# Performance work log

Hardware: AMD Instinct MI355X
Metric: run time of the kernel (lower is better)

The kernel has to match this reference:

```python
import jax, jax.numpy as jnp
import numpy as np

B, S, D = 2, 2048, 1024
H, DH = 16, 64
EPS = 1e-5

def setup_inputs() -> dict:
    key = jax.random.key(0)
    ks = jax.random.split(key, 8)
    s = 0.02
    return {
        "x": jax.random.normal(ks[0], (B, S, D), dtype=jnp.float32),
        "ln_gamma": jnp.ones((D,), jnp.float32),
        "ln_beta": jnp.zeros((D,), jnp.float32),
        "wq": jax.random.normal(ks[1], (D, H * DH), jnp.float32) * s,
        "bq": jnp.zeros((H * DH,), jnp.float32),
        "wk": jax.random.normal(ks[2], (D, H * DH), jnp.float32) * s,
        "bk": jnp.zeros((H * DH,), jnp.float32),
        "wv": jax.random.normal(ks[3], (D, H * DH), jnp.float32) * s,
        "bv": jnp.zeros((H * DH,), jnp.float32),
        "wo": jax.random.normal(ks[4], (H * DH, D), jnp.float32) * s,
        "bo": jnp.zeros((D,), jnp.float32),
    }

def reference(x, ln_gamma, ln_beta, wq, bq, wk, bk, wv, bv, wo, bo):
    # Pre-LayerNorm over d_model
    mu = jnp.mean(x, axis=-1, keepdims=True)
    var = jnp.var(x, axis=-1, keepdims=True)
    xn = (x - mu) * jax.lax.rsqrt(var + EPS) * ln_gamma + ln_beta

    b, s, _ = xn.shape
    q = (xn @ wq + bq).reshape(b, s, H, DH)
    k = (xn @ wk + bk).reshape(b, s, H, DH)
    v = (xn @ wv + bv).reshape(b, s, H, DH)

    scale = jnp.sqrt(jnp.float32(DH))
    scores = jnp.einsum('bihd,bjhd->bhij', q, k) / scale  # [b,h,s,s]
    att = jax.nn.softmax(scores, axis=-1)
    out = jnp.einsum('bhij,bjhd->bihd', att, v).reshape(b, s, H * DH)
    return out @ wo + bo
```

## Files before the change

### kernel.cpp

```cpp
#include <hip/hip_runtime.h>
#include <math.h>

#define SEQ   2048
#define DM    1024
#define NHEAD 16
#define HD    64
#define NTOK  4096
#define EPS   1e-5f
#define SCALE_C 0.18033688f

typedef __attribute__((ext_vector_type(8))) short v8s;
typedef __attribute__((ext_vector_type(4))) float v4f;
typedef unsigned short ushort_t;

#define GLOAD16(g, l) __builtin_amdgcn_global_load_lds( \
    (const __attribute__((address_space(1))) unsigned int*)(g), \
    (__attribute__((address_space(3))) unsigned int*)(l), 16, 0, 0)

__device__ __forceinline__ unsigned short f2bf(float f) {
  union { float f; unsigned u; } v; v.f = f;
  unsigned r = v.u + 0x7FFFu + ((v.u >> 16) & 1u);
  return (unsigned short)(r >> 16);
}

__device__ __forceinline__ unsigned pack2_bf16(float a, float b) {
  union { float f; unsigned u; } ua, ub;
  ua.f = a; ub.f = b;
  return __builtin_amdgcn_perm(ub.u + 0x8000u, ua.u + 0x8000u, 0x07060302u);
}

__global__ __launch_bounds__(256) void prep_kernel(
    const float* __restrict__ x, const float* __restrict__ g,
    const float* __restrict__ be, ushort_t* __restrict__ y,
    const float* __restrict__ w0, const float* __restrict__ w1,
    const float* __restrict__ w2, const float* __restrict__ w3,
    ushort_t* __restrict__ o0, ushort_t* __restrict__ o1,
    ushort_t* __restrict__ o2, ushort_t* __restrict__ o3) {
  __shared__ float tile[64][65];
  const int t = threadIdx.x;
  if (blockIdx.x < NTOK) {
    const int row = blockIdx.x;
    const float4 v = ((const float4*)(x + (size_t)row * DM))[t];
    float s  = v.x + v.y + v.z + v.w;
    float ss = v.x*v.x + v.y*v.y + v.z*v.z + v.w*v.w;
    #pragma unroll
    for (int off = 32; off > 0; off >>= 1) {
      s  += __shfl_down(s,  off, 64);
      ss += __shfl_down(ss, off, 64);
    }
    float* red = &tile[0][0];
    const int wid = t >> 6, lane = t & 63;
    if (lane == 0) { red[wid] = s; red[4 + wid] = ss; }
    __syncthreads();
    if (t == 0) {
      const float S  = red[0] + red[1] + red[2] + red[3];
      const float SS = red[4] + red[5] + red[6] + red[7];
      const float mu  = S * (1.0f / DM);
      const float var = SS * (1.0f / DM) - mu * mu;
      red[8] = mu; red[9] = rsqrtf(var + EPS);
    }
    __syncthreads();
    const float mu = red[8], r = red[9];
    const float4 gv = ((const float4*)g)[t];
    const float4 bv = ((const float4*)be)[t];
    ushort4 o;
    o.x = f2bf((v.x - mu) * r * gv.x + bv.x);
    o.y = f2bf((v.y - mu) * r * gv.y + bv.y);
    o.z = f2bf((v.z - mu) * r * gv.z + bv.z);
    o.w = f2bf((v.w - mu) * r * gv.w + bv.w);
    *(ushort4*)(y + (size_t)row * DM + t * 4) = o;
  } else {
    const int w = blockIdx.x - NTOK;
    const int z = w >> 8;
    const float* wp = (z==0) ? w0 : (z==1) ? w1 : (z==2) ? w2 : w3;
    ushort_t* o    = (z==0) ? o0 : (z==1) ? o1 : (z==2) ? o2 : o3;
    const int n0 = (w & 15) * 64, k0 = ((w >> 4) & 15) * 64;
    const int r = t >> 4, c4 = (t & 15) * 4;
    #pragma unroll
    for (int i = 0; i < 4; ++i) {
      const float4 v = *(const float4*)(wp + (size_t)(k0 + r + i*16) * DM + n0 + c4);
      tile[r + i*16][c4 + 0] = v.x;
      tile[r + i*16][c4 + 1] = v.y;
      tile[r + i*16][c4 + 2] = v.z;
      tile[r + i*16][c4 + 3] = v.w;
    }
    __syncthreads();
    #pragma unroll
    for (int i = 0; i < 4; ++i) {
      const int n = r + i*16;
      ushort4 o4;
      o4.x = f2bf(tile[c4 + 0][n]);
      o4.y = f2bf(tile[c4 + 1][n]);
      o4.z = f2bf(tile[c4 + 2][n]);
      o4.w = f2bf(tile[c4 + 3][n]);
      *(ushort4*)(o + (size_t)(n0 + n) * DM + k0 + c4) = o4;
    }
  }
}

__device__ __forceinline__ void gemm_main(ushort_t* lsa, ushort_t* lsb,
    const ushort_t* A, const ushort_t* WT, int m0, int n0, v4f acc[4][4]) {
  const int tid = threadIdx.x;
  const int wid = tid >> 6, lane = tid & 63;
  const int mh = (wid & 1) << 6, nh = (wid >> 1) << 6;
  const int r16 = lane & 15, quad = lane >> 4;
  const int srow = lane >> 2, sch = lane & 3;
  for (int k0 = 0; k0 < DM; k0 += 32) {
    __syncthreads();
    #pragma unroll
    for (int j = 0; j < 2; ++j) {
      const int o = wid * 2 + j;
      GLOAD16(A  + (size_t)(m0 + o*16 + srow) * DM + k0 + sch*8, lsa + o*512);
      GLOAD16(WT + (size_t)(n0 + o*16 + srow) * DM + k0 + sch*8, lsb + o*512);
    }
    __syncthreads();
    v8s af[4], bfr[4];
    #pragma unroll
    for (int i = 0; i < 4; ++i) {
      af[i]  = *(const v8s*)(lsa + (mh + i*16 + r16)*32 + quad*8);
      bfr[i] = *(const v8s*)(lsb + (nh + i*16 + r16)*32 + quad*8);
    }
    #pragma unroll
    for (int i = 0; i < 4; ++i)
      #pragma unroll
      for (int j = 0; j < 4; ++j)
        acc[i][j] = __builtin_amdgcn_mfma_f32_16x16x32_bf16(af[i], bfr[j], acc[i][j], 0, 0, 0);
  }
}

__global__ __launch_bounds__(256, 3) void gemm_qkv(const ushort_t* __restrict__ xn,
    const ushort_t* __restrict__ wtq, const ushort_t* __restrict__ wtk, const ushort_t* __restrict__ wtv,
    const float* __restrict__ bq, const float* __restrict__ bk, const float* __restrict__ bv,
    ushort_t* __restrict__ qo, ushort_t* __restrict__ ko, ushort_t* __restrict__ vto) {
  __shared__ ushort_t lsa[128*32];
  __shared__ ushort_t lsb[128*32];
  const int z = blockIdx.z;
  const ushort_t* WT = (z == 0) ? wtq : (z == 1) ? wtk : wtv;
  const float* bias  = (z == 0) ? bq  : (z == 1) ? bk  : bv;
  const int m0 = blockIdx.y * 128, n0 = blockIdx.x * 128;
  v4f acc[4][4];
  #pragma unroll
  for (int i = 0; i < 4; ++i)
    #pragma unroll
    for (int j = 0; j < 4; ++j) acc[i][j] = (v4f){0.f, 0.f, 0.f, 0.f};
  gemm_main(lsa, lsb, xn, WT, m0, n0, acc);
  const int tid = threadIdx.x, wid = tid >> 6, lane = tid & 63;
  const int mh = (wid & 1) << 6, nh = (wid >> 1) << 6;
  const int r16 = lane & 15, quad = lane >> 4;
  if (z < 2) {
    ushort_t* out = (z == 0) ? qo : ko;
    const float sc = (z == 0) ? SCALE_C : 1.0f;
    #pragma unroll
    for (int bn = 0; bn < 4; ++bn) {
      const int col = n0 + nh + bn*16 + r16;
      const float bb = bias[col];
      #pragma unroll
      for (int am = 0; am < 4; ++am) {
        const int tb = m0 + mh + am*16 + quad*4;
        #pragma unroll
        for (int r = 0; r < 4; ++r)
          out[(size_t)(tb + r) * DM + col] = f2bf((acc[am][bn][r] + bb) * sc);
      }
    }
  } else {
    #pragma unroll
    for (int bn = 0; bn < 4; ++bn) {
      const int col = n0 + nh + bn*16 + r16;
      const float bb = bias[col];
      const int h = col >> 6, d = col & 63;
      #pragma unroll
      for (int am = 0; am < 4; ++am) {
        const int tb = m0 + mh + am*16 + quad*4;
        const int b = tb >> 11, t = tb & 2047;
        ushort4 o4;
        o4.x = f2bf(acc[am][bn][0] + bb);
        o4.y = f2bf(acc[am][bn][1] + bb);
        o4.z = f2bf(acc[am][bn][2] + bb);
        o4.w = f2bf(acc[am][bn][3] + bb);
        *(ushort4*)(vto + ((size_t)(b*NHEAD + h) * HD + d) * SEQ + t) = o4;
      }
    }
  }
}

__global__ __launch_bounds__(256, 3) void gemm_out(const ushort_t* __restrict__ A,
    const ushort_t* __restrict__ WT, const float* __restrict__ bias,
    float* __restrict__ out) {
  __shared__ ushort_t lsa[128*32];
  __shared__ ushort_t lsb[128*32];
  const int m0 = blockIdx.y * 128, n0 = blockIdx.x * 128;
  v4f acc[4][4];
  #pragma unroll
  for (int i = 0; i < 4; ++i)
    #pragma unroll
    for (int j = 0; j < 4; ++j) acc[i][j] = (v4f){0.f, 0.f, 0.f, 0.f};
  gemm_main(lsa, lsb, A, WT, m0, n0, acc);
  const int tid = threadIdx.x, wid = tid >> 6, lane = tid & 63;
  const int mh = (wid & 1) << 6, nh = (wid >> 1) << 6;
  const int r16 = lane & 15, quad = lane >> 4;
  #pragma unroll
  for (int bn = 0; bn < 4; ++bn) {
    const int col = n0 + nh + bn*16 + r16;
    const float bb = bias[col];
    #pragma unroll
    for (int am = 0; am < 4; ++am) {
      const int tb = m0 + mh + am*16 + quad*4;
      #pragma unroll
      for (int r = 0; r < 4; ++r)
        out[(size_t)(tb + r) * DM + col] = acc[am][bn][r] + bb;
    }
  }
}

__global__ __launch_bounds__(256, 4) void attn_kernel(
    const ushort_t* __restrict__ Q, const ushort_t* __restrict__ K,
    const ushort_t* __restrict__ Vt, ushort_t* __restrict__ O) {
  __shared__ ushort_t pbuf[2][8*512];
  __shared__ float    lred[4][64];
  const int tid = threadIdx.x, wid = tid >> 6, lane = tid & 63;
  const int r16 = lane & 15, quad = lane >> 4;
  const int q0 = blockIdx.x * 64, bh = blockIdx.y;
  const int b = bh >> 4, h = bh & 15;
  const ushort_t* gQ = Q + (size_t)b * SEQ * DM + h * HD;
  const ushort_t* gK = K + (size_t)b * SEQ * DM + h * HD;
  const ushort_t* gV = Vt + (size_t)bh * HD * SEQ;

  v8s qfr[4][2];
  #pragma unroll
  for (int qa = 0; qa < 4; ++qa) {
    const ushort_t* p = gQ + (size_t)(q0 + qa*16 + r16) * DM + quad * 8;
    qfr[qa][0] = *(const v8s*)p;
    qfr[qa][1] = *(const v8s*)(p + 32);
  }
  v4f acco[4];
  #pragma unroll
  for (int i = 0; i < 4; ++i) acco[i] = (v4f){0.f, 0.f, 0.f, 0.f};
  float lrun[4] = {0.f, 0.f, 0.f, 0.f};

  const ushort_t* kp = gK + (size_t)(wid*16 + r16) * DM + quad * 8;
  const ushort_t* vp = gV + (size_t)(wid*16 + r16) * SEQ + quad * 8;

  const int pwoff = ((wid & 1) * 2 + (quad >> 1)) * 128 + r16 * 8 + (quad & 1) * 4;
  const int pblk0 = (wid >> 1) * 512;

  v8s kc0 = *(const v8s*)kp, kc1 = *(const v8s*)(kp + 32);
  v8s vc0 = *(const v8s*)vp, vc1 = *(const v8s*)(vp + 32);
  kp += 64 * DM; vp += 64;

  for (int kt = 0; kt < SEQ / 64; ++kt) {
    v8s kn0, kn1, vn0, vn1;
    if (kt + 1 < SEQ / 64) {
      kn0 = *(const v8s*)kp; kn1 = *(const v8s*)(kp + 32);
      vn0 = *(const v8s*)vp; vn1 = *(const v8s*)(vp + 32);
      kp += 64 * DM; vp += 64;
    }

    v4f sacc[4];
    #pragma unroll
    for (int qa = 0; qa < 4; ++qa) {
      sacc[qa] = (v4f){0.f, 0.f, 0.f, 0.f};
      sacc[qa] = __builtin_amdgcn_mfma_f32_16x16x32_bf16(kc0, qfr[qa][0], sacc[qa], 0, 0, 0);
      sacc[qa] = __builtin_amdgcn_mfma_f32_16x16x32_bf16(kc1, qfr[qa][1], sacc[qa], 0, 0, 0);
    }

    ushort_t* pw = pbuf[kt & 1];
    #pragma unroll
    for (int qa = 0; qa < 4; ++qa) {
      const float e0 = __builtin_amdgcn_exp2f(sacc[qa][0]);
      const float e1 = __builtin_amdgcn_exp2f(sacc[qa][1]);
      const float e2 = __builtin_amdgcn_exp2f(sacc[qa][2]);
      const float e3 = __builtin_amdgcn_exp2f(sacc[qa][3]);
      float ls = (e0 + e1) + (e2 + e3);
      ls += __shfl_xor(ls, 16, 64);
      ls += __shfl_xor(ls, 32, 64);
      lrun[qa] += ls;
      uint2 d2;
      d2.x = pack2_bf16(e0, e1);
      d2.y = pack2_bf16(e2, e3);
      *(uint2*)(pw + (qa*2) * 512 + pblk0 + pwoff) = d2;
    }

    __syncthreads();

    #pragma unroll
    for (int qa = 0; qa < 4; ++qa) {
      const v8s pb0 = *(const v8s*)(pw + (qa*2 + 0) * 512 + lane * 8);
      const v8s pb1 = *(const v8s*)(pw + (qa*2 + 1) * 512 + lane * 8);
      acco[qa] = __builtin_amdgcn_mfma_f32_16x16x32_bf16(vc0, pb0, acco[qa], 0, 0, 0);
      acco[qa] = __builtin_amdgcn_mfma_f32_16x16x32_bf16(vc1, pb1, acco[qa], 0, 0, 0);
    }

    kc0 = kn0; kc1 = kn1; vc0 = vn0; vc1 = vn1;
  }

  if (quad == 0) {
    #pragma unroll
    for (int qa = 0; qa < 4; ++qa) lred[wid][qa*16 + r16] = lrun[qa];
  }
  __syncthreads();
  ushort_t* gO = O + (size_t)b * SEQ * DM + h * HD;
  #pragma unroll
  for (int qa = 0; qa < 4; ++qa) {
    const int q = qa*16 + r16;
    const float inv = 1.f / ((lred[0][q] + lred[1][q]) + (lred[2][q] + lred[3][q]));
    ushort4 o4;
    o4.x = f2bf(acco[qa][0] * inv);
    o4.y = f2bf(acco[qa][1] * inv);
    o4.z = f2bf(acco[qa][2] * inv);
    o4.w = f2bf(acco[qa][3] * inv);
    *(ushort4*)(gO + (size_t)(q0 + q) * DM + wid*16 + quad*4) = o4;
  }
}

extern "C" void kernel_launch(void* const* d_in, const int* in_sizes, int n_in,
                              void* d_out, int out_size, void* d_ws, size_t ws_size,
                              hipStream_t stream) {
  const float* x     = (const float*)d_in[0];
  const float* gamma = (const float*)d_in[1];
  const float* beta  = (const float*)d_in[2];
  const float* wq    = (const float*)d_in[3];
  const float* bq    = (const float*)d_in[4];
  const float* wk    = (const float*)d_in[5];
  const float* bk    = (const float*)d_in[6];
  const float* wv    = (const float*)d_in[7];
  const float* bv    = (const float*)d_in[8];
  const float* wo    = (const float*)d_in[9];
  const float* bo    = (const float*)d_in[10];
  float* out = (float*)d_out;

  unsigned char* w8 = (unsigned char*)d_ws;
  const size_t MB = 1024 * 1024;
  ushort_t* xn  = (ushort_t*)(w8 + 0 * MB);
  ushort_t* qb  = (ushort_t*)(w8 + 8 * MB);
  ushort_t* kb  = (ushort_t*)(w8 + 16 * MB);
  ushort_t* vt  = (ushort_t*)(w8 + 24 * MB);
  ushort_t* wtq = (ushort_t*)(w8 + 32 * MB);
  ushort_t* wtk = (ushort_t*)(w8 + 34 * MB);
  ushort_t* wtv = (ushort_t*)(w8 + 36 * MB);
  ushort_t* wto = (ushort_t*)(w8 + 38 * MB);
  ushort_t* ob  = xn;

  prep_kernel<<<dim3(NTOK + 1024), dim3(256), 0, stream>>>(
      x, gamma, beta, xn, wq, wk, wv, wo, wtq, wtk, wtv, wto);
  gemm_qkv<<<dim3(8, 32, 3), dim3(256), 0, stream>>>(xn, wtq, wtk, wtv, bq, bk, bv, qb, kb, vt);
  attn_kernel<<<dim3(SEQ / 64, 2 * NHEAD), dim3(256), 0, stream>>>(qb, kb, vt, ob);
  gemm_out<<<dim3(8, 32, 1), dim3(256), 0, stream>>>(ob, wto, bo, out);
}
```

Before: 216.1 us.

## Keep P in registers and split PV over keys per wave, reducing at end

New measurement: 253.9 us. +17.5%, slower.

```diff
diff --git a/kernel.cpp b/kernel.cpp
--- a/kernel.cpp
+++ b/kernel.cpp
@@ -10,6 +10,7 @@
 #define SCALE_C 0.18033688f
 
 typedef __attribute__((ext_vector_type(8))) short v8s;
+typedef __attribute__((ext_vector_type(4))) short v4s;
 typedef __attribute__((ext_vector_type(4))) float v4f;
 typedef unsigned short ushort_t;
 
@@ -28,6 +29,18 @@
   ua.f = a; ub.f = b;
   return __builtin_amdgcn_perm(ub.u + 0x8000u, ua.u + 0x8000u, 0x07060302u);
 }
+
+#if __has_builtin(__builtin_amdgcn_mfma_f32_16x16x16bf16_1k)
+__device__ __forceinline__ v4f pv_mfma(v4s a, v4s b, v4f c) {
+  return __builtin_amdgcn_mfma_f32_16x16x16bf16_1k(a, b, c, 0, 0, 0);
+}
+#else
+__device__ __forceinline__ v4f pv_mfma(v4s a, v4s b, v4f c) {
+  v8s a8 = (v8s){a[0], a[1], a[2], a[3], 0, 0, 0, 0};
+  v8s b8 = (v8s){b[0], b[1], b[2], b[3], 0, 0, 0, 0};
+  return __builtin_amdgcn_mfma_f32_16x16x32_bf16(a8, b8, c, 0, 0, 0);
+}
+#endif
 
 __global__ __launch_bounds__(256) void prep_kernel(
     const float* __restrict__ x, const float* __restrict__ g,
@@ -212,11 +225,11 @@
   }
 }
 
-__global__ __launch_bounds__(256, 4) void attn_kernel(
+__global__ __launch_bounds__(256, 3) void attn_kernel(
     const ushort_t* __restrict__ Q, const ushort_t* __restrict__ K,
     const ushort_t* __restrict__ Vt, ushort_t* __restrict__ O) {
-  __shared__ ushort_t pbuf[2][8*512];
-  __shared__ float    lred[4][64];
+  __shared__ float obuf[4][16][65];
+  __shared__ float lred[4][64];
   const int tid = threadIdx.x, wid = tid >> 6, lane = tid & 63;
   const int r16 = lane & 15, quad = lane >> 4;
   const int q0 = blockIdx.x * 64, bh = blockIdx.y;
@@ -232,27 +245,24 @@
     qfr[qa][0] = *(const v8s*)p;
     qfr[qa][1] = *(const v8s*)(p + 32);
   }
-  v4f acco[4];
-  #pragma unroll
-  for (int i = 0; i < 4; ++i) acco[i] = (v4f){0.f, 0.f, 0.f, 0.f};
+  v4f acco[4][4];
+  #pragma unroll
+  for (int i = 0; i < 4; ++i)
+    #pragma unroll
+    for (int j = 0; j < 4; ++j) acco[i][j] = (v4f){0.f, 0.f, 0.f, 0.f};
   float lrun[4] = {0.f, 0.f, 0.f, 0.f};
 
   const ushort_t* kp = gK + (size_t)(wid*16 + r16) * DM + quad * 8;
-  const ushort_t* vp = gV + (size_t)(wid*16 + r16) * SEQ + quad * 8;
-
-  const int pwoff = ((wid & 1) * 2 + (quad >> 1)) * 128 + r16 * 8 + (quad & 1) * 4;
-  const int pblk0 = (wid >> 1) * 512;
+  const ushort_t* vp = gV + (size_t)r16 * SEQ + wid*16 + quad*4;
 
   v8s kc0 = *(const v8s*)kp, kc1 = *(const v8s*)(kp + 32);
-  v8s vc0 = *(const v8s*)vp, vc1 = *(const v8s*)(vp + 32);
-  kp += 64 * DM; vp += 64;
+  kp += (size_t)64 * DM;
 
   for (int kt = 0; kt < SEQ / 64; ++kt) {
-    v8s kn0, kn1, vn0, vn1;
+    v8s kn0, kn1;
     if (kt + 1 < SEQ / 64) {
       kn0 = *(const v8s*)kp; kn1 = *(const v8s*)(kp + 32);
-      vn0 = *(const v8s*)vp; vn1 = *(const v8s*)(vp + 32);
-      kp += 64 * DM; vp += 64;
+      kp += (size_t)64 * DM;
     }
 
     v4f sacc[4];
@@ -263,52 +273,80 @@
       sacc[qa] = __builtin_amdgcn_mfma_f32_16x16x32_bf16(kc1, qfr[qa][1], sacc[qa], 0, 0, 0);
     }
 
-    ushort_t* pw = pbuf[kt & 1];
+    v4s pfr[4];
     #pragma unroll
     for (int qa = 0; qa < 4; ++qa) {
       const float e0 = __builtin_amdgcn_exp2f(sacc[qa][0]);
       const float e1 = __builtin_amdgcn_exp2f(sacc[qa][1]);
       const float e2 = __builtin_amdgcn_exp2f(sacc[qa][2]);
       const float e3 = __builtin_amdgcn_exp2f(sacc[qa][3]);
-      float ls = (e0 + e1) + (e2 + e3);
-      ls += __shfl_xor(ls, 16, 64);
-      ls += __shfl_xor(ls, 32, 64);
-      lrun[qa] += ls;
-      uint2 d2;
-      d2.x = pack2_bf16(e0, e1);
-      d2.y = pack2_bf16(e2, e3);
-      *(uint2*)(pw + (qa*2) * 512 + pblk0 + pwoff) = d2;
-    }
-
-    __syncthreads();
-
-    #pragma unroll
-    for (int qa = 0; qa < 4; ++qa) {
-      const v8s pb0 = *(const v8s*)(pw + (qa*2 + 0) * 512 + lane * 8);
-      const v8s pb1 = *(const v8s*)(pw + (qa*2 + 1) * 512 + lane * 8);
-      acco[qa] = __builtin_amdgcn_mfma_f32_16x16x32_bf16(vc0, pb0, acco[qa], 0, 0, 0);
-      acco[qa] = __builtin_amdgcn_mfma_f32_16x16x32_bf16(vc1, pb1, acco[qa], 0, 0, 0);
-    }
-
-    kc0 = kn0; kc1 = kn1; vc0 = vn0; vc1 = vn1;
-  }
-
+      lrun[qa] += (e0 + e1) + (e2 + e3);
+      union { unsigned u[2]; v4s s; } pk;
+      pk.u[0] = pack2_bf16(e0, e1);
+      pk.u[1] = pack2_bf16(e2, e3);
+      pfr[qa] = pk.s;
+    }
+
+    #pragma unroll
+    for (int dg = 0; dg < 4; ++dg) {
+      const v4s vf = *(const v4s*)(vp + (size_t)(dg*16) * SEQ);
+      #pragma unroll
+      for (int qa = 0; qa < 4; ++qa)
+        acco[dg][qa] = pv_mfma(vf, pfr[qa], acco[dg][qa]);
+    }
+    vp += 64;
+
+    kc0 = kn0; kc1 = kn1;
+  }
+
+  #pragma unroll
+  for (int qa = 0; qa < 4; ++qa) {
+    lrun[qa] += __shfl_xor(lrun[qa], 16, 64);
+    lrun[qa] += __shfl_xor(lrun[qa], 32, 64);
+  }
   if (quad == 0) {
     #pragma unroll
     for (int qa = 0; qa < 4; ++qa) lred[wid][qa*16 + r16] = lrun[qa];
   }
   __syncthreads();
-  ushort_t* gO = O + (size_t)b * SEQ * DM + h * HD;
+  float inv[4];
   #pragma unroll
   for (int qa = 0; qa < 4; ++qa) {
     const int q = qa*16 + r16;
-    const float inv = 1.f / ((lred[0][q] + lred[1][q]) + (lred[2][q] + lred[3][q]));
-    ushort4 o4;
-    o4.x = f2bf(acco[qa][0] * inv);
-    o4.y = f2bf(acco[qa][1] * inv);
-    o4.z = f2bf(acco[qa][2] * inv);
-    o4.w = f2bf(acco[qa][3] * inv);
-    *(ushort4*)(gO + (size_t)(q0 + q) * DM + wid*16 + quad*4) = o4;
+    inv[qa] = 1.f / ((lred[0][q] + lred[1][q]) + (lred[2][q] + lred[3][q]));
+  }
+
+  ushort_t* gO = O + (size_t)b * SEQ * DM + h * HD;
+  for (int sg = 0; sg < 4; ++sg) {
+    #pragma unroll
+    for (int qa = 0; qa < 4; ++qa)
+      #pragma unroll
+      for (int r = 0; r < 4; ++r)
+        obuf[wid][quad*4 + r][qa*16 + r16] = acco[sg][qa][r];
+    __syncthreads();
+    if (wid == sg) {
+      #pragma unroll
+      for (int qa = 0; qa < 4; ++qa) {
+        const int q = qa*16 + r16;
+        float s0 = acco[sg][qa][0], s1 = acco[sg][qa][1];
+        float s2 = acco[sg][qa][2], s3 = acco[sg][qa][3];
+        #pragma unroll
+        for (int w = 0; w < 4; ++w) {
+          if (w == sg) continue;
+          s0 += obuf[w][quad*4 + 0][q];
+          s1 += obuf[w][quad*4 + 1][q];
+          s2 += obuf[w][quad*4 + 2][q];
+          s3 += obuf[w][quad*4 + 3][q];
+        }
+        ushort4 o4;
+        o4.x = f2bf(s0 * inv[qa]);
+        o4.y = f2bf(s1 * inv[qa]);
+        o4.z = f2bf(s2 * inv[qa]);
+        o4.w = f2bf(s3 * inv[qa]);
+        *(ushort4*)(gO + (size_t)(q0 + q) * DM + sg*16 + quad*4) = o4;
+      }
+    }
+    __syncthreads();
   }
 }
 
```
